# Kernel tuning notes

Hardware: AMD Instinct MI355X
Metric: run time of the kernel (lower is better)

Reference implementation:

```python
import jax, jax.numpy as jnp
import numpy as np

E, C, K, S = 8, 128, 512, 512  # embedding_dim, channels, kernel_size, stride
NEG_SLOPE = 0.01  # torch F.leaky_relu default


def setup_inputs() -> dict:
    key = jax.random.key(0)
    ks = jax.random.split(key, 11)
    B, T = 4, 1_000_000
    sc = 0.05
    return {
        "x": jax.random.normal(ks[0], (B, T, E), jnp.float32),
        # ctx_conv: Conv1d(E, 2C, K, stride=S) -> weight (2C, E, K), bias (2C,)
        "ctx_conv_w": jax.random.normal(ks[1], (2 * C, E, K), jnp.float32) * sc,
        "ctx_conv_b": jax.random.normal(ks[2], (2 * C,), jnp.float32) * sc,
        # ctx_share: Conv1d(C, C, 1) -> (C, C) pointwise
        "ctx_share_w": jax.random.normal(ks[3], (C, C), jnp.float32) * sc,
        "ctx_share_b": jax.random.normal(ks[4], (C,), jnp.float32) * sc,
        "main_conv_w": jax.random.normal(ks[5], (2 * C, E, K), jnp.float32) * sc,
        "main_conv_b": jax.random.normal(ks[6], (2 * C,), jnp.float32) * sc,
        "main_share_w": jax.random.normal(ks[7], (C, C), jnp.float32) * sc,
        "main_share_b": jax.random.normal(ks[8], (C,), jnp.float32) * sc,
        # gct_proj: Linear(C, C) -> weight (C, C) (y = g @ W.T + b)
        "gct_proj_w": jax.random.normal(ks[9], (C, C), jnp.float32) * sc,
        "gct_proj_b": jax.random.normal(ks[10], (C,), jnp.float32) * sc,
    }


def _leaky(x):
    return jnp.where(x >= 0, x, NEG_SLOPE * x)


def _glu(x):  # GLU over channel dim 1
    a, b = jnp.split(x, 2, axis=1)
    return a * jax.nn.sigmoid(b)


def _conv(z, w, b):
    # z: (B, Cin, T), w: (Cout, Cin, K) -> (B, Cout, T_out), stride S, VALID
    y = jax.lax.conv_general_dilated(z, w, (S,), 'VALID',
                                     dimension_numbers=('NCH', 'OIH', 'NCH'))
    return y + b[None, :, None]


def _branch_act(z, wc, bc, ws, bs):
    # glu(conv(z)) -> leaky_relu(1x1 share conv)
    h = _glu(_conv(z, wc, bc))                                   # (B, C, T_out)
    h = _leaky(jnp.einsum('oc,bct->bot', ws, h) + bs[None, :, None])
    return h


def reference(x, ctx_conv_w, ctx_conv_b, ctx_share_w, ctx_share_b,
              main_conv_w, main_conv_b, main_share_w, main_share_b,
              gct_proj_w, gct_proj_b):
    z = jnp.transpose(x, (0, 2, 1))  # (B, E, T)
    # Context branch: global max over time of ctx activations (GCG context).
    g = _branch_act(z, ctx_conv_w, ctx_conv_b, ctx_share_w, ctx_share_b)
    gct = jnp.max(g, axis=-1)  # (B, C)
    # Main branch with global channel gating.
    h = _branch_act(z, main_conv_w, main_conv_b, main_share_w, main_share_b)  # (B, C, T_out)
    q = jnp.tanh(gct @ gct_proj_w.T + gct_proj_b)                # (B, C)
    gate = jax.nn.sigmoid(jnp.einsum('bct,bc->bt', h, q))        # (B, T_out)
    out = jnp.max(h * gate[:, None, :], axis=-1)                 # (B, C)
    return out
```

## Files before the change

kernel.cpp:

```cpp
#include <hip/hip_runtime.h>
#include <hip/hip_bf16.h>
#include <cmath>

#define B_    4
#define T_    1000000
#define E_    8
#define C_    128
#define NCH   512
#define KK    4096
#define TOUT  1953
#define TP    1956
#define NT2   31

typedef __attribute__((ext_vector_type(8))) short bf16x8;
typedef __attribute__((ext_vector_type(4))) float f32x4;

__device__ __forceinline__ float sigmoidf_(float v) { return 1.f / (1.f + __expf(-v)); }

__device__ __forceinline__ void gload_lds16(const __hip_bfloat16* g, __hip_bfloat16* l) {
  __builtin_amdgcn_global_load_lds(
      (const __attribute__((address_space(1))) void*)(const void*)g,
      (__attribute__((address_space(3))) void*)(void*)l, 16, 0, 0);
}

#define MEMFENCE() asm volatile("" ::: "memory")

__global__ __launch_bounds__(256) void prep_inputs(
    const float* __restrict__ wc, const float* __restrict__ bc,
    const float* __restrict__ wm, const float* __restrict__ bm,
    __hip_bfloat16* __restrict__ Wn2, float* __restrict__ bias_t) {
  __shared__ float row[KK];
  const int n = blockIdx.x, br = n >> 8, o = n & 255;
  const float* wsrc = (br ? wm : wc) + (size_t)o * KK;
  for (int i = threadIdx.x; i < KK; i += 256) row[i] = wsrc[i];
  __syncthreads();
  const int nt = n >> 4, nr = n & 15;
  for (int k = threadIdx.x; k < KK; k += 256) {
    int kpos = k >> 3, e = k & 7;
    size_t addr = (((size_t)nt * 128 + (k >> 5)) * 64
                   + (size_t)((k >> 3) & 3) * 16 + nr) * 8 + (k & 7);
    Wn2[addr] = __float2bfloat16(row[e * 512 + kpos]);
  }
  if (threadIdx.x == 0) bias_t[n] = (br ? bm : bc)[o];
}

__global__ __launch_bounds__(512, 2) void mfma_gemm(
    const float* __restrict__ x, const __hip_bfloat16* __restrict__ Wn2,
    float* __restrict__ u2) {
  __shared__ __hip_bfloat16 Bs[4][8192];

  const int tid  = threadIdx.x;
  const int lane = tid & 63, wave = tid >> 6;
  const int wt = wave & 3, wn = wave >> 2;

  const int L   = blockIdx.x;
  const int xcd = L & 7;
  const int r   = L >> 3;
  const int nb  = r & 3;
  const int sh  = r >> 2;
  const int s   = sh * 8 + xcd;
  const int tblk = s & 15, b = s >> 4;
  const int t0 = tblk * 128, n0 = nb * 128;

  int rA0 = t0 + wt * 32 + (lane & 15);
  int rA1 = rA0 + 16;
  if (rA0 >= TOUT) rA0 = 0;
  if (rA1 >= TOUT) rA1 = 0;
  const int kA = (lane >> 4) * 8;
  const float* pA0 = x + (size_t)b * 8000000ull + (size_t)rA0 * KK + kA;
  const float* pA1 = x + (size_t)b * 8000000ull + (size_t)rA1 * KK + kA;

  const __hip_bfloat16* gB = Wn2 + ((size_t)(nb * 8 + wave) * 128) * 512
                             + (size_t)lane * 8;

  f32x4 acc[2][4];
#pragma unroll
  for (int i = 0; i < 2; ++i)
#pragma unroll
    for (int j = 0; j < 4; ++j) acc[i][j] = (f32x4)(0.0f);

  float4 Ar0[2][2][2], Ar1[2][2][2];
  bf16x8 aF[2][2], bF[4][2];

  auto ALOAD = [&](float4 (&Ar)[2][2][2], int step) {
#pragma unroll
    for (int i = 0; i < 2; ++i) {
      const float* p = (i ? pA1 : pA0) + (size_t)step * 64;
#pragma unroll
      for (int c = 0; c < 2; ++c) {
        Ar[i][c][0] = *(const float4*)(p + c * 32);
        Ar[i][c][1] = *(const float4*)(p + c * 32 + 4);
      }
    }
  };
  auto ACVT = [&](float4 (&Ar)[2][2][2]) {
#pragma unroll
    for (int i = 0; i < 2; ++i)
#pragma unroll
      for (int c = 0; c < 2; ++c) {
        union { __hip_bfloat16 h[8]; bf16x8 v; } u;
        float4 lo = Ar[i][c][0], hi = Ar[i][c][1];
        u.h[0] = __float2bfloat16(lo.x); u.h[1] = __float2bfloat16(lo.y);
        u.h[2] = __float2bfloat16(lo.z); u.h[3] = __float2bfloat16(lo.w);
        u.h[4] = __float2bfloat16(hi.x); u.h[5] = __float2bfloat16(hi.y);
        u.h[6] = __float2bfloat16(hi.z); u.h[7] = __float2bfloat16(hi.w);
        aF[i][c] = u.v;
      }
  };
  auto BSTAGE = [&](int buf, int step) {
    const __hip_bfloat16* g = gB + (size_t)step * 1024;
    gload_lds16(g,       &Bs[buf][(size_t)(wave * 2) * 512]);
    gload_lds16(g + 512, &Bs[buf][(size_t)(wave * 2 + 1) * 512]);
  };
  auto BREAD = [&](int buf) {
#pragma unroll
    for (int j = 0; j < 4; ++j)
#pragma unroll
      for (int c = 0; c < 2; ++c)
        bF[j][c] = *(const bf16x8*)(&Bs[buf][(size_t)((wn * 4 + j) * 2 + c) * 512
                                             + (size_t)lane * 8]);
  };
  auto MFMA16 = [&]() {
#pragma unroll
    for (int c = 0; c < 2; ++c)
#pragma unroll
      for (int i = 0; i < 2; ++i)
#pragma unroll
        for (int j = 0; j < 4; ++j)
          acc[i][j] = __builtin_amdgcn_mfma_f32_16x16x32_bf16(aF[i][c], bF[j][c],
                                                              acc[i][j], 0, 0, 0);
  };

  BSTAGE(0, 0);
  MEMFENCE();
  ALOAD(Ar0, 0);
  MEMFENCE();
  BSTAGE(1, 1);
  MEMFENCE();
  ALOAD(Ar1, 1);
  asm volatile("s_waitcnt vmcnt(18)" ::: "memory");
  __builtin_amdgcn_sched_barrier(0);
  asm volatile("s_barrier" ::: "memory");

#pragma unroll 1
  for (int it = 0; it < 16; ++it) {
    const int t4 = it * 4;
#pragma unroll
    for (int u = 0; u < 4; ++u) {
      BSTAGE((u + 2) & 3, t4 + u + 2);
      asm volatile("s_waitcnt vmcnt(12)" ::: "memory");
      __builtin_amdgcn_sched_barrier(0);
      if ((u & 1) == 0) { ACVT(Ar0); ALOAD(Ar0, t4 + u + 2); }
      else              { ACVT(Ar1); ALOAD(Ar1, t4 + u + 2); }
      BREAD(u);
      __builtin_amdgcn_s_setprio(1);
      MFMA16();
      __builtin_amdgcn_s_setprio(0);
      asm volatile("s_waitcnt vmcnt(18)" ::: "memory");
      __builtin_amdgcn_sched_barrier(0);
      asm volatile("s_barrier" ::: "memory");
    }
  }

  const int crow = (lane >> 4) * 4;
  const int ccol = lane & 15;
#pragma unroll
  for (int j = 0; j < 4; ++j) {
    int n = n0 + wn * 64 + j * 16 + ccol;
    float* urow = u2 + ((size_t)n * B_ + b) * TP;
#pragma unroll
    for (int i = 0; i < 2; ++i) {
      int t = t0 + wt * 32 + i * 16 + crow;
      if (t < TOUT) *(f32x4*)(urow + t) = acc[i][j];
    }
  }
}

__global__ __launch_bounds__(256) void share_act(
    const float* __restrict__ u2, const float* __restrict__ bias_t,
    const float* __restrict__ wsc, const float* __restrict__ bsc,
    const float* __restrict__ wsm, const float* __restrict__ bsm,
    float* __restrict__ hmain, float* __restrict__ gct_part) {
  __shared__ float Wl[128 * 132];
  __shared__ float ul[128 * 68];
  const int tid  = threadIdx.x;
  const int tile = blockIdx.x;
  const int b    = blockIdx.y;
  const int br   = blockIdx.z;
  const int t0   = tile * 64;
  const float* ws = br ? wsm : wsc;
  const float* bs = br ? bsm : bsc;

  for (int g = tid; g < 16384; g += 256) {
    int co = g >> 7, cp = g & 127;
    Wl[cp * 132 + co] = ws[g];
  }
  const size_t base_v = ((size_t)(br * 256) * B_ + b) * TP;
  const size_t base_g = ((size_t)(br * 256 + 128) * B_ + b) * TP;
  for (int g = tid; g < 8192; g += 256) {
    int cp = g >> 6, t = g & 63;
    float v = 0.f;
    if (t0 + t < TOUT) {
      float va = u2[base_v + (size_t)cp * B_ * TP + t0 + t] + bias_t[br * 256 + cp];
      float vg = u2[base_g + (size_t)cp * B_ * TP + t0 + t] + bias_t[br * 256 + 128 + cp];
      v = va * sigmoidf_(vg);
    }
    ul[cp * 68 + t] = v;
  }
  __syncthreads();

  const int ty = tid >> 4, tx = tid & 15;
  float acc[8][4];
#pragma unroll
  for (int i = 0; i < 8; ++i)
#pragma unroll
    for (int j = 0; j < 4; ++j) acc[i][j] = 0.f;

  for (int cp = 0; cp < 128; ++cp) {
    float4 a0 = *(const float4*)&Wl[cp*132 + ty*4];
    float4 a1 = *(const float4*)&Wl[cp*132 + 64 + ty*4];
    float4 b4 = *(const float4*)&ul[cp*68 + tx*4];
    float av[8] = {a0.x,a0.y,a0.z,a0.w,a1.x,a1.y,a1.z,a1.w};
    float bv[4] = {b4.x,b4.y,b4.z,b4.w};
#pragma unroll
    for (int i = 0; i < 8; ++i)
#pragma unroll
      for (int j = 0; j < 4; ++j) acc[i][j] = fmaf(av[i], bv[j], acc[i][j]);
  }

  float mloc[8];
#pragma unroll
  for (int i = 0; i < 8; ++i) mloc[i] = -INFINITY;
#pragma unroll
  for (int i = 0; i < 8; ++i) {
    int c = (i < 4) ? (ty*4 + i) : (64 + ty*4 + (i - 4));
    float bias = bs[c];
#pragma unroll
    for (int j = 0; j < 4; ++j) {
      int t = t0 + tx*4 + j;
      if (t >= TOUT) continue;
      float v = acc[i][j] + bias;
      v = (v >= 0.f) ? v : 0.01f * v;
      if (br == 1) {
        hmain[((size_t)b * 128 + c) * TOUT + t] = v;
      } else {
        mloc[i] = fmaxf(mloc[i], v);
      }
    }
  }
  if (br == 0) {
    __syncthreads();
    float* red = ul;
#pragma unroll
    for (int i = 0; i < 8; ++i) {
      int c = (i < 4) ? (ty*4 + i) : (64 + ty*4 + (i - 4));
      red[c * 16 + tx] = mloc[i];
    }
    __syncthreads();
    if (tid < 128) {
      float m = -INFINITY;
#pragma unroll
      for (int k = 0; k < 16; ++k) m = fmaxf(m, red[tid * 16 + k]);
      gct_part[((size_t)b * 128 + tid) * NT2 + tile] = m;
    }
  }
}

__global__ void gct_q(const float* __restrict__ gct_part, const float* __restrict__ wp,
                      const float* __restrict__ bp, float* __restrict__ q) {
  int b = blockIdx.x, tid = threadIdx.x;
  __shared__ float g[128];
  float m = -INFINITY;
  for (int tl = 0; tl < NT2; ++tl) m = fmaxf(m, gct_part[((size_t)b * 128 + tid) * NT2 + tl]);
  g[tid] = m;
  __syncthreads();
  float s = bp[tid];
  for (int c = 0; c < 128; ++c) s = fmaf(g[c], wp[tid * 128 + c], s);
  q[b * 128 + tid] = tanhf(s);
}

__global__ __launch_bounds__(256) void gate_max(
    const float* __restrict__ hmain, const float* __restrict__ q,
    float* __restrict__ out_part) {
  __shared__ float hl[128 * 68];
  __shared__ float ql[128];
  __shared__ float red[256];
  __shared__ float gl[64];
  int tid = threadIdx.x, tile = blockIdx.x, b = blockIdx.y;
  int t0 = tile * 64;
  for (int g = tid; g < 8192; g += 256) {
    int c = g >> 6, t = g & 63;
    hl[c * 68 + t] = (t0 + t < TOUT) ? hmain[((size_t)b * 128 + c) * TOUT + t0 + t] : 0.f;
  }
  if (tid < 128) ql[tid] = q[b * 128 + tid];
  __syncthreads();
  {
    int t = tid & 63, cy = tid >> 6;
    float s = 0.f;
#pragma unroll
    for (int cc = 0; cc < 32; ++cc) s = fmaf(hl[(cy * 32 + cc) * 68 + t], ql[cy * 32 + cc], s);
    red[cy * 64 + t] = s;
  }
  __syncthreads();
  if (tid < 64) {
    float s = red[tid] + red[64 + tid] + red[128 + tid] + red[192 + tid];
    gl[tid] = sigmoidf_(s);
  }
  __syncthreads();
  {
    int c = tid >> 1, th = tid & 1;
    float m = -INFINITY;
#pragma unroll
    for (int tt = 0; tt < 32; ++tt) {
      int t = th * 32 + tt;
      if (t0 + t < TOUT) m = fmaxf(m, hl[c * 68 + t] * gl[t]);
    }
    red[c * 2 + th] = m;
  }
  __syncthreads();
  if (tid < 128) out_part[((size_t)b * 128 + tid) * NT2 + tile] = fmaxf(red[tid * 2], red[tid * 2 + 1]);
}

__global__ void final_max(const float* __restrict__ out_part, float* __restrict__ out) {
  int idx = blockIdx.x * 256 + threadIdx.x;
  if (idx < 512) {
    float m = -INFINITY;
    for (int tl = 0; tl < NT2; ++tl) m = fmaxf(m, out_part[(size_t)idx * NT2 + tl]);
    out[idx] = m;
  }
}

extern "C" void kernel_launch(void* const* d_in, const int* in_sizes, int n_in,
                              void* d_out, int out_size, void* d_ws, size_t ws_size,
                              hipStream_t stream) {
  const float* x      = (const float*)d_in[0];
  const float* ctx_w  = (const float*)d_in[1];
  const float* ctx_b  = (const float*)d_in[2];
  const float* ctx_sw = (const float*)d_in[3];
  const float* ctx_sb = (const float*)d_in[4];
  const float* main_w = (const float*)d_in[5];
  const float* main_b = (const float*)d_in[6];
  const float* main_sw= (const float*)d_in[7];
  const float* main_sb= (const float*)d_in[8];
  const float* gp_w   = (const float*)d_in[9];
  const float* gp_b   = (const float*)d_in[10];

  char* w = (char*)d_ws;
  __hip_bfloat16* Wn2 = (__hip_bfloat16*)(w);
  float* bias_t  = (float*)(w + 4194304);
  float* u2      = (float*)(w + 4196352);
  float* hmain   = (float*)(w + 20219904);
  float* gct_part= (float*)(w + 24219648);
  float* q       = (float*)(w + 24283136);
  float* out_part= (float*)(w + 24285184);

  prep_inputs<<<NCH, 256, 0, stream>>>(ctx_w, ctx_b, main_w, main_b, Wn2, bias_t);
  mfma_gemm<<<256, 512, 0, stream>>>(x, Wn2, u2);
  share_act<<<dim3(NT2, B_, 2), 256, 0, stream>>>(u2, bias_t, ctx_sw, ctx_sb,
                                                  main_sw, main_sb, hmain, gct_part);
  gct_q<<<B_, 128, 0, stream>>>(gct_part, gp_w, gp_b, q);
  gate_max<<<dim3(NT2, B_), 256, 0, stream>>>(hmain, q, out_part);
  final_max<<<2, 256, 0, stream>>>(out_part, (float*)d_out);
}
```

Measured before the change: 375.6 us.

## Load B fragments directly to registers, drop LDS staging and barriers

Removes the LDS staging of weight fragments via global_load_lds and the per-step block barriers in the MFMA GEMM. Each wave now loads its own B fragments straight from global memory into registers, using a 4-deep register prefetch ring over 32-wide K steps. This avoids LDS traffic and block-wide sync. In exchange, each weight fragment is fetched by every wave that uses it (redundant global/L2 traffic across the 4 wt waves), register pressure rises, and the loop now relies on compiler-scheduled waits instead of explicit vmcnt control. The final iteration also prefetches past the end of K (steps 128–131), which reads beyond each row's bounds.

```diff
diff --git a/kernel.cpp b/kernel.cpp
--- a/kernel.cpp
+++ b/kernel.cpp
@@ -17,14 +17,6 @@
 
 __device__ __forceinline__ float sigmoidf_(float v) { return 1.f / (1.f + __expf(-v)); }
 
-__device__ __forceinline__ void gload_lds16(const __hip_bfloat16* g, __hip_bfloat16* l) {
-  __builtin_amdgcn_global_load_lds(
-      (const __attribute__((address_space(1))) void*)(const void*)g,
-      (__attribute__((address_space(3))) void*)(void*)l, 16, 0, 0);
-}
-
-#define MEMFENCE() asm volatile("" ::: "memory")
-
 __global__ __launch_bounds__(256) void prep_inputs(
     const float* __restrict__ wc, const float* __restrict__ bc,
     const float* __restrict__ wm, const float* __restrict__ bm,
@@ -47,8 +39,6 @@
 __global__ __launch_bounds__(512, 2) void mfma_gemm(
     const float* __restrict__ x, const __hip_bfloat16* __restrict__ Wn2,
     float* __restrict__ u2) {
-  __shared__ __hip_bfloat16 Bs[4][8192];
-
   const int tid  = threadIdx.x;
   const int lane = tid & 63, wave = tid >> 6;
   const int wt = wave & 3, wn = wave >> 2;
@@ -70,8 +60,10 @@
   const float* pA0 = x + (size_t)b * 8000000ull + (size_t)rA0 * KK + kA;
   const float* pA1 = x + (size_t)b * 8000000ull + (size_t)rA1 * KK + kA;
 
-  const __hip_bfloat16* gB = Wn2 + ((size_t)(nb * 8 + wave) * 128) * 512
-                             + (size_t)lane * 8;
+  const __hip_bfloat16* gB[4];
+#pragma unroll
+  for (int j = 0; j < 4; ++j)
+    gB[j] = Wn2 + ((size_t)(nb * 8 + wn * 4 + j) * 128) * 512 + (size_t)lane * 8;
 
   f32x4 acc[2][4];
 #pragma unroll
@@ -79,88 +71,61 @@
 #pragma unroll
     for (int j = 0; j < 4; ++j) acc[i][j] = (f32x4)(0.0f);
 
-  float4 Ar0[2][2][2], Ar1[2][2][2];
-  bf16x8 aF[2][2], bF[4][2];
-
-  auto ALOAD = [&](float4 (&Ar)[2][2][2], int step) {
-#pragma unroll
-    for (int i = 0; i < 2; ++i) {
-      const float* p = (i ? pA1 : pA0) + (size_t)step * 64;
-#pragma unroll
-      for (int c = 0; c < 2; ++c) {
-        Ar[i][c][0] = *(const float4*)(p + c * 32);
-        Ar[i][c][1] = *(const float4*)(p + c * 32 + 4);
-      }
-    }
-  };
-  auto ACVT = [&](float4 (&Ar)[2][2][2]) {
-#pragma unroll
-    for (int i = 0; i < 2; ++i)
-#pragma unroll
-      for (int c = 0; c < 2; ++c) {
-        union { __hip_bfloat16 h[8]; bf16x8 v; } u;
-        float4 lo = Ar[i][c][0], hi = Ar[i][c][1];
-        u.h[0] = __float2bfloat16(lo.x); u.h[1] = __float2bfloat16(lo.y);
-        u.h[2] = __float2bfloat16(lo.z); u.h[3] = __float2bfloat16(lo.w);
-        u.h[4] = __float2bfloat16(hi.x); u.h[5] = __float2bfloat16(hi.y);
-        u.h[6] = __float2bfloat16(hi.z); u.h[7] = __float2bfloat16(hi.w);
-        aF[i][c] = u.v;
-      }
-  };
-  auto BSTAGE = [&](int buf, int step) {
-    const __hip_bfloat16* g = gB + (size_t)step * 1024;
-    gload_lds16(g,       &Bs[buf][(size_t)(wave * 2) * 512]);
-    gload_lds16(g + 512, &Bs[buf][(size_t)(wave * 2 + 1) * 512]);
-  };
-  auto BREAD = [&](int buf) {
-#pragma unroll
-    for (int j = 0; j < 4; ++j)
-#pragma unroll
-      for (int c = 0; c < 2; ++c)
-        bF[j][c] = *(const bf16x8*)(&Bs[buf][(size_t)((wn * 4 + j) * 2 + c) * 512
-                                             + (size_t)lane * 8]);
-  };
-  auto MFMA16 = [&]() {
-#pragma unroll
-    for (int c = 0; c < 2; ++c)
-#pragma unroll
-      for (int i = 0; i < 2; ++i)
-#pragma unroll
-        for (int j = 0; j < 4; ++j)
-          acc[i][j] = __builtin_amdgcn_mfma_f32_16x16x32_bf16(aF[i][c], bF[j][c],
-                                                              acc[i][j], 0, 0, 0);
-  };
-
-  BSTAGE(0, 0);
-  MEMFENCE();
-  ALOAD(Ar0, 0);
-  MEMFENCE();
-  BSTAGE(1, 1);
-  MEMFENCE();
-  ALOAD(Ar1, 1);
-  asm volatile("s_waitcnt vmcnt(18)" ::: "memory");
-  __builtin_amdgcn_sched_barrier(0);
-  asm volatile("s_barrier" ::: "memory");
+  float4 Ar[4][2][2];
+  bf16x8 Br[4][4];
+
+#define LOADSET(SET, SS)                                                  \
+  do {                                                                    \
+    const int ss_ = (SS);                                                 \
+    const float* p0_ = pA0 + (size_t)ss_ * 32;                            \
+    const float* p1_ = pA1 + (size_t)ss_ * 32;                            \
+    Ar[SET][0][0] = *(const float4*)(p0_);                                \
+    Ar[SET][0][1] = *(const float4*)(p0_ + 4);                            \
+    Ar[SET][1][0] = *(const float4*)(p1_);                                \
+    Ar[SET][1][1] = *(const float4*)(p1_ + 4);                            \
+    Br[SET][0] = *(const bf16x8*)(gB[0] + (size_t)ss_ * 512);             \
+    Br[SET][1] = *(const bf16x8*)(gB[1] + (size_t)ss_ * 512);             \
+    Br[SET][2] = *(const bf16x8*)(gB[2] + (size_t)ss_ * 512);             \
+    Br[SET][3] = *(const bf16x8*)(gB[3] + (size_t)ss_ * 512);             \
+  } while (0)
+
+#define CVTMFMA(SET)                                                      \
+  do {                                                                    \
+    bf16x8 aF_[2];                                                        \
+    _Pragma("unroll")                                                     \
+    for (int i_ = 0; i_ < 2; ++i_) {                                      \
+      union { __hip_bfloat16 h[8]; bf16x8 v; } u_;                        \
+      float4 lo_ = Ar[SET][i_][0], hi_ = Ar[SET][i_][1];                  \
+      u_.h[0] = __float2bfloat16(lo_.x); u_.h[1] = __float2bfloat16(lo_.y); \
+      u_.h[2] = __float2bfloat16(lo_.z); u_.h[3] = __float2bfloat16(lo_.w); \
+      u_.h[4] = __float2bfloat16(hi_.x); u_.h[5] = __float2bfloat16(hi_.y); \
+      u_.h[6] = __float2bfloat16(hi_.z); u_.h[7] = __float2bfloat16(hi_.w); \
+      aF_[i_] = u_.v;                                                     \
+    }                                                                     \
+    _Pragma("unroll")                                                     \
+    for (int i_ = 0; i_ < 2; ++i_)                                        \
+      _Pragma("unroll")                                                   \
+      for (int j_ = 0; j_ < 4; ++j_)                                      \
+        acc[i_][j_] = __builtin_amdgcn_mfma_f32_16x16x32_bf16(            \
+            aF_[i_], Br[SET][j_], acc[i_][j_], 0, 0, 0);                  \
+  } while (0)
+
+  LOADSET(0, 0);
+  LOADSET(1, 1);
+  LOADSET(2, 2);
+  LOADSET(3, 3);
 
 #pragma unroll 1
-  for (int it = 0; it < 16; ++it) {
-    const int t4 = it * 4;
-#pragma unroll
-    for (int u = 0; u < 4; ++u) {
-      BSTAGE((u + 2) & 3, t4 + u + 2);
-      asm volatile("s_waitcnt vmcnt(12)" ::: "memory");
-      __builtin_amdgcn_sched_barrier(0);
-      if ((u & 1) == 0) { ACVT(Ar0); ALOAD(Ar0, t4 + u + 2); }
-      else              { ACVT(Ar1); ALOAD(Ar1, t4 + u + 2); }
-      BREAD(u);
-      __builtin_amdgcn_s_setprio(1);
-      MFMA16();
-      __builtin_amdgcn_s_setprio(0);
-      asm volatile("s_waitcnt vmcnt(18)" ::: "memory");
-      __builtin_amdgcn_sched_barrier(0);
-      asm volatile("s_barrier" ::: "memory");
-    }
-  }
+  for (int it = 0; it < 32; ++it) {
+    const int base = it * 4;
+    CVTMFMA(0); LOADSET(0, base + 4);
+    CVTMFMA(1); LOADSET(1, base + 5);
+    CVTMFMA(2); LOADSET(2, base + 6);
+    CVTMFMA(3); LOADSET(3, base + 7);
+  }
+
+#undef LOADSET
+#undef CVTMFMA
 
   const int crow = (lane >> 4) * 4;
   const int ccol = lane & 15;
```

After: 424.8 us. 13.1% more time.
